# Performance work log

Measured on AMD Instinct MI355X. Metric: run time of the kernel, lower is better.

## Reference

```python
import jax, jax.numpy as jnp
import numpy as np

HEADS1, HID1 = 4, 64   # layer 1: concat -> 256
HEADS2, HID2 = 1, 64   # layer 2: out_channels
NEG_SLOPE = 0.2


def gat_layer(x_src, x_dst, W_src, W_dst, att_src, att_dst, bias, src, dst, n_tgt, heads, hid):
    # bipartite GATConv (PyG math), concat heads
    xs = (x_src @ W_src).reshape(-1, heads, hid)          # [Ns,H,C]
    xd = (x_dst @ W_dst).reshape(-1, heads, hid)          # [Nt,H,C]
    a_s = jnp.sum(xs * att_src, axis=-1)                  # [Ns,H]
    a_d = jnp.sum(xd * att_dst, axis=-1)                  # [Nt,H]
    e = jax.nn.leaky_relu(a_s[src] + a_d[dst], NEG_SLOPE) # [E,H]
    m = jax.ops.segment_max(e, dst, num_segments=n_tgt)
    m = jnp.where(jnp.isfinite(m), m, 0.0)
    ex = jnp.exp(e - m[dst])
    denom = jax.ops.segment_sum(ex, dst, num_segments=n_tgt)
    alpha = ex / (denom[dst] + 1e-16)                     # edge softmax per target
    msg = xs[src] * alpha[:, :, None]                     # [E,H,C]
    out = jax.ops.segment_sum(msg, dst, num_segments=n_tgt)
    return out.reshape(n_tgt, heads * hid) + bias


def setup_inputs() -> dict:
    key = jax.random.key(0)
    ks = jax.random.split(key, 20)
    N0, NT1, NT2 = 100000, 25000, 5000
    E1, E2 = 400000, 100000
    IN, H1 = 256, HEADS1 * HID1  # 256
    OUT = HEADS2 * HID2          # 64
    g = lambda k, sh, fan: jax.random.normal(k, sh, jnp.float32) * (1.0 / np.sqrt(fan))
    return {
        'x': jax.random.normal(ks[0], (N0, IN), jnp.float32),
        'src1': jax.random.randint(ks[1], (E1,), 0, N0),
        'dst1': jax.random.randint(ks[2], (E1,), 0, NT1),
        'src2': jax.random.randint(ks[3], (E2,), 0, NT1),
        'dst2': jax.random.randint(ks[4], (E2,), 0, NT2),
        'n_tgt1': NT1, 'n_tgt2': NT2,
        'W1_src': g(ks[5], (IN, H1), IN), 'W1_dst': g(ks[6], (IN, H1), IN),
        'att1_src': g(ks[7], (HEADS1, HID1), HID1), 'att1_dst': g(ks[8], (HEADS1, HID1), HID1),
        'bias1': jnp.zeros((H1,), jnp.float32),
        'skip1_W': g(ks[9], (IN, H1), IN), 'skip1_b': jnp.zeros((H1,), jnp.float32),
        'W2_src': g(ks[10], (H1, OUT), H1), 'W2_dst': g(ks[11], (H1, OUT), H1),
        'att2_src': g(ks[12], (HEADS2, HID2), HID2), 'att2_dst': g(ks[13], (HEADS2, HID2), HID2),
        'bias2': jnp.zeros((OUT,), jnp.float32),
        'skip2_W': g(ks[14], (H1, OUT), H1), 'skip2_b': jnp.zeros((OUT,), jnp.float32),
    }


def reference(x, src1, dst1, src2, dst2, n_tgt1, n_tgt2,
              W1_src, W1_dst, att1_src, att1_dst, bias1, skip1_W, skip1_b,
              W2_src, W2_dst, att2_src, att2_dst, bias2, skip2_W, skip2_b):
    # layer 1: conv + skip + elu (dropout inactive in eval)
    x_t1 = x[:n_tgt1]
    h = gat_layer(x, x_t1, W1_src, W1_dst, att1_src, att1_dst, bias1,
                  src1, dst1, n_tgt1, HEADS1, HID1)
    h = h + (x_t1 @ skip1_W + skip1_b)
    h = jax.nn.elu(h)
    # layer 2 (final): conv + skip, then log_softmax
    x_t2 = h[:n_tgt2]
    o = gat_layer(h, x_t2, W2_src, W2_dst, att2_src, att2_dst, bias2,
                  src2, dst2, n_tgt2, HEADS2, HID2)
    o = o + (x_t2 @ skip2_W + skip2_b)
    return jax.nn.log_softmax(o, axis=-1)
```

## Files before the change

kernel.cpp:

```cpp
#include <hip/hip_runtime.h>
#include <hip/hip_bf16.h>

using bf16 = __hip_bfloat16;
typedef __attribute__((ext_vector_type(8))) short short8;
typedef __attribute__((ext_vector_type(4))) short short4v;
typedef __attribute__((ext_vector_type(4))) float float4v;

__device__ __forceinline__ short f2bs(float x) {
    bf16 b = __float2bfloat16(x);
    return __builtin_bit_cast(short, b);
}
__device__ __forceinline__ float bs2f(short s) {
    return __uint_as_float(((unsigned)(unsigned short)s) << 16);
}
__device__ __forceinline__ void glds16(const void* g, void* l) {
    __builtin_amdgcn_global_load_lds(
        (const __attribute__((address_space(1))) unsigned int*)g,
        (__attribute__((address_space(3))) unsigned int*)l, 16, 0, 0);
}

__global__ __launch_bounds__(512, 4) void gemm_l1(
        const float* __restrict__ A, const bf16* __restrict__ Bt,
        bf16* __restrict__ xs1, bf16* __restrict__ sk1,
        float* __restrict__ as1, float* __restrict__ ad1,
        const float* __restrict__ att_s, const float* __restrict__ att_d,
        int M, int NT) {
    __shared__ short ldsB[64 * 512];
    const int y = blockIdx.y;
    const int row0 = blockIdx.x * 128;
    if (y >= 2 && row0 >= NT) return;
    const int col0 = y * 128;
    const int tid = threadIdx.x;
    const int wave = tid >> 6, lane = tid & 63;
    const int quad = lane >> 4, l16 = lane & 15;

#pragma unroll
    for (int kit = 0; kit < 8; kit++)
        glds16(&Bt[(size_t)(col0 + wave * 16 + l16) * 256 + kit * 32 + quad * 8],
               &ldsB[(wave * 8 + kit) * 512]);

    const int arow_ = row0 + wave * 16 + l16;
    const int arow = arow_ < M ? arow_ : M - 1;
    const float* Ap = &A[(size_t)arow * 256 + quad * 8];

    const float4v fz = {0.f, 0.f, 0.f, 0.f};
    float4v acc[8];
#pragma unroll
    for (int n = 0; n < 8; n++) acc[n] = fz;

    __syncthreads();

    float4v pf0[4], pf1[4];
#pragma unroll
    for (int i = 0; i < 4; i++) {
        pf0[i] = *(const float4v*)(Ap + i * 32);
        pf1[i] = *(const float4v*)(Ap + i * 32 + 4);
    }

#pragma unroll
    for (int kit = 0; kit < 8; kit++) {
        const int s = kit & 3;
        short8 af;
#pragma unroll
        for (int j = 0; j < 4; j++) { af[j] = f2bs(pf0[s][j]); af[4 + j] = f2bs(pf1[s][j]); }
        if (kit < 4) {
            pf0[s] = *(const float4v*)(Ap + (kit + 4) * 32);
            pf1[s] = *(const float4v*)(Ap + (kit + 4) * 32 + 4);
        }
#pragma unroll
        for (int n = 0; n < 8; n++) {
            short8 bf = *(short8*)&ldsB[(n * 8 + kit) * 512 + lane * 8];
            acc[n] = __builtin_amdgcn_mfma_f32_16x16x32_bf16(af, bf, acc[n], 0, 0, 0);
        }
    }

    const int rbase = row0 + wave * 16 + quad * 4;

    if (y < 4) {
        const float* attc = y < 2 ? att_s : att_d;
        const int hbase = y < 2 ? y * 2 : (y - 2) * 2;
        const int aM = y < 2 ? M : NT;
        float* aout = y < 2 ? as1 : ad1;
#pragma unroll
        for (int h = 0; h < 2; h++) {
            float av[4];
#pragma unroll
            for (int n = 0; n < 4; n++) av[n] = attc[(hbase + h) * 64 + n * 16 + l16];
#pragma unroll
            for (int r = 0; r < 4; r++) {
                float t = acc[h * 4 + 0][r] * av[0] + acc[h * 4 + 1][r] * av[1] +
                          acc[h * 4 + 2][r] * av[2] + acc[h * 4 + 3][r] * av[3];
                t += __shfl_xor(t, 1, 64);
                t += __shfl_xor(t, 2, 64);
                t += __shfl_xor(t, 4, 64);
                t += __shfl_xor(t, 8, 64);
                int grow = rbase + r;
                if (l16 == 0 && grow < aM) aout[(size_t)grow * 4 + hbase + h] = t;
            }
        }
    }

    if (y < 2) {
#pragma unroll
        for (int n = 0; n < 8; n++) {
            int col = col0 + n * 16 + l16;
#pragma unroll
            for (int r = 0; r < 4; r++) {
                int row = rbase + r;
                if (row < M) xs1[(size_t)row * 256 + col] = __float2bfloat16(acc[n][r]);
            }
        }
    } else if (y >= 4) {
#pragma unroll
        for (int n = 0; n < 8; n++) {
            int scol = col0 - 512 + n * 16 + l16;
#pragma unroll
            for (int r = 0; r < 4; r++) {
                int row = rbase + r;
                if (row < NT) sk1[(size_t)row * 256 + scol] = __float2bfloat16(acc[n][r]);
            }
        }
    }
}

__global__ __launch_bounds__(512, 4) void gemm_l2(
        const bf16* __restrict__ Ah, const bf16* __restrict__ Bt,
        float* __restrict__ x2, float* __restrict__ a2,
        const float* __restrict__ attc, int NT) {
    __shared__ short ldsB[32 * 512];
    const int y = blockIdx.y;
    const int row0 = blockIdx.x * 128;
    const int col0 = y * 64;
    const int tid = threadIdx.x;
    const int wave = tid >> 6, lane = tid & 63;
    const int quad = lane >> 4, l16 = lane & 15;

#pragma unroll
    for (int i = 0; i < 4; i++) {
        int blk = wave * 4 + i;
        int cb = blk >> 3, kit = blk & 7;
        glds16(&Bt[(size_t)(col0 + cb * 16 + l16) * 256 + kit * 32 + quad * 8],
               &ldsB[blk * 512]);
    }

    const int arow = row0 + wave * 16 + l16;
    const bf16* Ap = &Ah[(size_t)arow * 256 + quad * 8];

    const float4v fz = {0.f, 0.f, 0.f, 0.f};
    float4v acc[4];
#pragma unroll
    for (int n = 0; n < 4; n++) acc[n] = fz;

    __syncthreads();

    short8 s[8];
#pragma unroll
    for (int kit = 0; kit < 8; kit++) s[kit] = *(const short8*)(Ap + kit * 32);

#pragma unroll
    for (int kit = 0; kit < 8; kit++) {
#pragma unroll
        for (int n = 0; n < 4; n++) {
            short8 bf = *(short8*)&ldsB[(n * 8 + kit) * 512 + lane * 8];
            acc[n] = __builtin_amdgcn_mfma_f32_16x16x32_bf16(s[kit], bf, acc[n], 0, 0, 0);
        }
    }

    const int rbase = row0 + wave * 16 + quad * 4;

    if (y < 2) {
        float av[4];
#pragma unroll
        for (int n = 0; n < 4; n++) av[n] = attc[y * 64 + n * 16 + l16];
#pragma unroll
        for (int r = 0; r < 4; r++) {
            float t = acc[0][r] * av[0] + acc[1][r] * av[1] +
                      acc[2][r] * av[2] + acc[3][r] * av[3];
            t += __shfl_xor(t, 1, 64);
            t += __shfl_xor(t, 2, 64);
            t += __shfl_xor(t, 4, 64);
            t += __shfl_xor(t, 8, 64);
            int grow = rbase + r;
            if (l16 == 0 && grow < NT) a2[(size_t)grow * 2 + y] = t;
        }
    }
#pragma unroll
    for (int n = 0; n < 4; n++) {
        int col = col0 + n * 16 + l16;
#pragma unroll
        for (int r = 0; r < 4; r++) {
            int row = rbase + r;
            if (row < NT) x2[(size_t)row * 192 + col] = acc[n][r];
        }
    }
}

__global__ void prep_all(const float* __restrict__ W1s, const float* __restrict__ W1d,
                         const float* __restrict__ W1sk, const float* __restrict__ W2s,
                         const float* __restrict__ W2d, const float* __restrict__ W2sk,
                         const float* __restrict__ a2s, const float* __restrict__ a2d,
                         bf16* __restrict__ Wt1, bf16* __restrict__ Wt2,
                         float* __restrict__ at2c, int* __restrict__ fills, int nfill) {
    int t = blockIdx.x * blockDim.x + threadIdx.x;
    if (t < 196608) {
        int n = t >> 8, k = t & 255;
        const float* W = n < 256 ? W1s : (n < 512 ? W1d : W1sk);
        Wt1[t] = __float2bfloat16(W[k * 256 + (n & 255)]);
    } else if (t < 245760) {
        int i = t - 196608;
        int n = i >> 8, k = i & 255;
        const float* W = n < 64 ? W2s : (n < 128 ? W2d : W2sk);
        Wt2[i] = __float2bfloat16(W[k * 64 + (n & 63)]);
    } else if (t < 245888) {
        int i = t - 245760;
        at2c[i] = i < 64 ? a2s[i] : a2d[i - 64];
    } else if (t < 245888 + nfill) {
        fills[t - 245888] = 0;
    }
}

__global__ void bucket_scatter(const int* __restrict__ s1, const int* __restrict__ d1, int E1,
                               const int* __restrict__ s2, const int* __restrict__ d2, int E2,
                               int* __restrict__ fill1, int* __restrict__ fill2,
                               int* __restrict__ psrc1, int* __restrict__ psrc2) {
    int t = blockIdx.x * blockDim.x + threadIdx.x;
    if (t < E1) {
        int d = d1[t];
        int pos = atomicAdd(&fill1[d], 1);
        if (pos < 64) psrc1[(d << 6) + pos] = s1[t];
    } else if (t < E1 + E2) {
        int tt = t - E1;
        int d = d2[tt];
        int pos = atomicAdd(&fill2[d], 1);
        if (pos < 64) psrc2[(d << 6) + pos] = s2[tt];
    }
}

__global__ __launch_bounds__(256) void agg_h4(
        const int* __restrict__ fill, const int* __restrict__ psrc,
        const bf16* __restrict__ X, const float* __restrict__ as1,
        const float* __restrict__ ad1, const float* __restrict__ bias,
        const bf16* __restrict__ skip, const float* __restrict__ skipb,
        bf16* __restrict__ h) {
    __shared__ float exl[4][64][4];
    __shared__ float red[4][256];
    const int d = blockIdx.x;
    const int tid = threadIdx.x;
    const int wv = tid >> 6, lane = tid & 63;
    const int head = lane >> 4;
    int deg = fill[d];
    deg = deg < 64 ? deg : 64;
    int se = 0;
    float4v ex4 = {0.f, 0.f, 0.f, 0.f};
    const float4v ad4 = *(const float4v*)&ad1[(size_t)d * 4];
    if (lane < deg) {
        se = psrc[((size_t)d << 6) + lane];
        float4v as4 = *(const float4v*)&as1[(size_t)se * 4];
#pragma unroll
        for (int c = 0; c < 4; c++) {
            float v = as4[c] + ad4[c];
            v = v > 0.f ? v : 0.2f * v;
            ex4[c] = expf(v);
        }
    }
    *(float4v*)&exl[wv][lane][0] = ex4;
    float4v dn = ex4;
#pragma unroll
    for (int o = 32; o; o >>= 1) {
        dn.x += __shfl_xor(dn.x, o, 64);
        dn.y += __shfl_xor(dn.y, o, 64);
        dn.z += __shfl_xor(dn.z, o, 64);
        dn.w += __shfl_xor(dn.w, o, 64);
    }
    float4v acc = {0.f, 0.f, 0.f, 0.f}, acc2 = {0.f, 0.f, 0.f, 0.f};
    int p = wv;
    for (; p + 4 < deg; p += 8) {
        int sA = __shfl(se, p, 64), sB = __shfl(se, p + 4, 64);
        float aA = exl[wv][p][head], aB = exl[wv][p + 4][head];
        short4v xa = *(const short4v*)&X[(size_t)sA * 256 + lane * 4];
        short4v xb = *(const short4v*)&X[(size_t)sB * 256 + lane * 4];
        acc.x += bs2f(xa.x) * aA; acc2.x += bs2f(xb.x) * aB;
        acc.y += bs2f(xa.y) * aA; acc2.y += bs2f(xb.y) * aB;
        acc.z += bs2f(xa.z) * aA; acc2.z += bs2f(xb.z) * aB;
        acc.w += bs2f(xa.w) * aA; acc2.w += bs2f(xb.w) * aB;
    }
    for (; p < deg; p += 4) {
        int sA = __shfl(se, p, 64);
        float aA = exl[wv][p][head];
        short4v xa = *(const short4v*)&X[(size_t)sA * 256 + lane * 4];
        acc.x += bs2f(xa.x) * aA;
        acc.y += bs2f(xa.y) * aA;
        acc.z += bs2f(xa.z) * aA;
        acc.w += bs2f(xa.w) * aA;
    }
    acc.x += acc2.x; acc.y += acc2.y; acc.z += acc2.z; acc.w += acc2.w;
    *(float4v*)&red[wv][lane * 4] = acc;
    __syncthreads();
    const int f = tid;
    float sum = red[0][f] + red[1][f] + red[2][f] + red[3][f];
    int hf = f >> 6;
    float den = hf == 0 ? dn.x : hf == 1 ? dn.y : hf == 2 ? dn.z : dn.w;
    float v = sum / (den + 1e-16f) + bias[f] + __bfloat162float(skip[(size_t)d * 256 + f]) +
              skipb[f];
    h[(size_t)d * 256 + f] = __float2bfloat16(v > 0.f ? v : expm1f(v));
}

__global__ __launch_bounds__(256) void agg_h1(
        const int* __restrict__ fill2, const int* __restrict__ psrc2,
        const float* __restrict__ x2, const float* __restrict__ a2,
        const float* __restrict__ bias, const float* __restrict__ skipb,
        float* __restrict__ out, int M) {
    const int d = blockIdx.x * 4 + (threadIdx.x >> 6);
    const int lane = threadIdx.x & 63;
    if (d >= M) return;
    int deg = fill2[d];
    deg = deg < 64 ? deg : 64;
    int se = 0;
    float exv = 0.f;
    const float adv = a2[(size_t)d * 2 + 1];
    if (lane < deg) {
        se = psrc2[((size_t)d << 6) + lane];
        float v = a2[(size_t)se * 2] + adv;
        v = v > 0.f ? v : 0.2f * v;
        exv = expf(v);
    }
    float den = exv;
#pragma unroll
    for (int o = 32; o; o >>= 1) den += __shfl_xor(den, o, 64);
    float acc = 0.f, acc2 = 0.f;
    int p = 0;
    for (; p + 1 < deg; p += 2) {
        int sA = __shfl(se, p, 64), sB = __shfl(se, p + 1, 64);
        float aA = __shfl(exv, p, 64), aB = __shfl(exv, p + 1, 64);
        acc += x2[(size_t)sA * 192 + lane] * aA;
        acc2 += x2[(size_t)sB * 192 + lane] * aB;
    }
    if (p < deg) {
        int sA = __shfl(se, p, 64);
        acc += x2[(size_t)sA * 192 + lane] * __shfl(exv, p, 64);
    }
    float v = (acc + acc2) / (den + 1e-16f) + bias[lane] +
              x2[(size_t)d * 192 + 128 + lane] + skipb[lane];
    float m = v;
#pragma unroll
    for (int o = 32; o; o >>= 1) m = fmaxf(m, __shfl_xor(m, o, 64));
    float e = expf(v - m);
#pragma unroll
    for (int o = 32; o; o >>= 1) e += __shfl_xor(e, o, 64);
    out[(size_t)d * 64 + lane] = v - m - logf(e);
}

extern "C" void kernel_launch(void* const* d_in, const int* in_sizes, int n_in,
                              void* d_out, int out_size, void* d_ws, size_t ws_size,
                              hipStream_t stream) {
    const float* x        = (const float*)d_in[0];
    const int*   src1     = (const int*)d_in[1];
    const int*   dst1     = (const int*)d_in[2];
    const int*   src2     = (const int*)d_in[3];
    const int*   dst2     = (const int*)d_in[4];
    const float* W1_src   = (const float*)d_in[7];
    const float* W1_dst   = (const float*)d_in[8];
    const float* att1_src = (const float*)d_in[9];
    const float* att1_dst = (const float*)d_in[10];
    const float* bias1    = (const float*)d_in[11];
    const float* skip1_W  = (const float*)d_in[12];
    const float* skip1_b  = (const float*)d_in[13];
    const float* W2_src   = (const float*)d_in[14];
    const float* W2_dst   = (const float*)d_in[15];
    const float* att2_src = (const float*)d_in[16];
    const float* att2_dst = (const float*)d_in[17];
    const float* bias2    = (const float*)d_in[18];
    const float* skip2_W  = (const float*)d_in[19];
    const float* skip2_b  = (const float*)d_in[20];

    const int N0  = in_sizes[0] / 256;
    const int E1  = in_sizes[1];
    const int E2  = in_sizes[3];
    const int NT1 = 25000, NT2 = 5000;
    const int NT1p = 25088;

    char* ws = (char*)d_ws;
    size_t off = 0;
    auto alloc = [&](size_t b) { size_t o = off; off += (b + 255) & ~(size_t)255; return o; };
    size_t o_xs1   = alloc((size_t)N0 * 256 * 2);
    size_t o_sk1   = alloc((size_t)NT1 * 256 * 2);
    size_t o_h     = alloc((size_t)NT1p * 256 * 2);
    size_t o_as1   = alloc((size_t)N0 * 4 * 4);
    size_t o_ad1   = alloc((size_t)NT1 * 4 * 4);
    size_t o_fill  = alloc((size_t)(NT1 + NT2) * 4);
    size_t o_psrc1 = alloc((size_t)NT1 * 64 * 4);
    size_t o_psrc2 = alloc((size_t)NT2 * 64 * 4);
    size_t o_wt1   = alloc((size_t)768 * 256 * 2);
    size_t o_wt2   = alloc((size_t)192 * 256 * 2);
    size_t o_at2c  = alloc((size_t)128 * 4);
    size_t off2a = o_xs1;
    auto alloc2 = [&](size_t b) { size_t o = off2a; off2a += (b + 255) & ~(size_t)255; return o; };
    size_t o_x2 = alloc2((size_t)NT1 * 192 * 4);
    size_t o_a2 = alloc2((size_t)NT1 * 2 * 4);

    bf16*  xs1   = (bf16*)(ws + o_xs1);
    bf16*  sk1   = (bf16*)(ws + o_sk1);
    bf16*  h     = (bf16*)(ws + o_h);
    float* as1   = (float*)(ws + o_as1);
    float* ad1   = (float*)(ws + o_ad1);
    int*   fill1 = (int*)(ws + o_fill);
    int*   fill2 = fill1 + NT1;
    int*   psrc1 = (int*)(ws + o_psrc1);
    int*   psrc2 = (int*)(ws + o_psrc2);
    bf16*  Wt1   = (bf16*)(ws + o_wt1);
    bf16*  Wt2   = (bf16*)(ws + o_wt2);
    float* at2c  = (float*)(ws + o_at2c);
    float* x2    = (float*)(ws + o_x2);
    float* a2    = (float*)(ws + o_a2);

    prep_all<<<(245888 + NT1 + NT2 + 255) / 256, 256, 0, stream>>>(
        W1_src, W1_dst, skip1_W, W2_src, W2_dst, skip2_W, att2_src, att2_dst,
        Wt1, Wt2, at2c, fill1, NT1 + NT2);
    bucket_scatter<<<(E1 + E2 + 255) / 256, 256, 0, stream>>>(
        src1, dst1, E1, src2, dst2, E2, fill1, fill2, psrc1, psrc2);
    gemm_l1<<<dim3((N0 + 127) / 128, 6), 512, 0, stream>>>(
        x, Wt1, xs1, sk1, as1, ad1, att1_src, att1_dst, N0, NT1);
    agg_h4<<<NT1, 256, 0, stream>>>(fill1, psrc1, xs1, as1, ad1, bias1, sk1, skip1_b, h);
    gemm_l2<<<dim3((NT1 + 127) / 128, 3), 512, 0, stream>>>(h, Wt2, x2, a2, at2c, NT1);
    agg_h1<<<(NT2 + 3) / 4, 256, 0, stream>>>(fill2, psrc2, x2, a2, bias2, skip2_b,
                                              (float*)d_out, NT2);
}
```

Measured before the change: 351.1 us.

## Pre-convert x to bf16 and retile layer-1 GEMM to 64-column blocks

Adds a bf16 conversion of the input features x to a fused prep kernel, which also absorbs the edge bucket scatter and weight transposes. The fill counters are now zeroed with a memset. The layer-1 GEMM reads bf16 A directly, uses 64-column tiles across 12 column blocks with column-major grid ordering so blocks sharing A rows run together, and loads A fragments before the barrier. This cuts the GEMM's A-read traffic and per-block register and LDS use. In exchange it adds an extra 51MB bf16 write and read of x and a larger workspace.

```diff
diff --git a/kernel.cpp b/kernel.cpp
--- a/kernel.cpp
+++ b/kernel.cpp
@@ -20,89 +20,78 @@
 }
 
 __global__ __launch_bounds__(512, 4) void gemm_l1(
-        const float* __restrict__ A, const bf16* __restrict__ Bt,
+        const bf16* __restrict__ A, const bf16* __restrict__ Bt,
         bf16* __restrict__ xs1, bf16* __restrict__ sk1,
         float* __restrict__ as1, float* __restrict__ ad1,
         const float* __restrict__ att_s, const float* __restrict__ att_d,
         int M, int NT) {
-    __shared__ short ldsB[64 * 512];
-    const int y = blockIdx.y;
-    const int row0 = blockIdx.x * 128;
-    if (y >= 2 && row0 >= NT) return;
-    const int col0 = y * 128;
+    __shared__ short ldsB[32 * 512];
+    const int y = blockIdx.x;
+    const int row0 = blockIdx.y * 128;
+    if (y >= 4 && row0 >= NT) return;
+    const int col0 = y * 64;
     const int tid = threadIdx.x;
     const int wave = tid >> 6, lane = tid & 63;
     const int quad = lane >> 4, l16 = lane & 15;
 
 #pragma unroll
-    for (int kit = 0; kit < 8; kit++)
-        glds16(&Bt[(size_t)(col0 + wave * 16 + l16) * 256 + kit * 32 + quad * 8],
-               &ldsB[(wave * 8 + kit) * 512]);
+    for (int i = 0; i < 4; i++) {
+        int blk = wave * 4 + i;
+        int cb = blk >> 3, kit = blk & 7;
+        glds16(&Bt[(size_t)(col0 + cb * 16 + l16) * 256 + kit * 32 + quad * 8],
+               &ldsB[blk * 512]);
+    }
 
     const int arow_ = row0 + wave * 16 + l16;
     const int arow = arow_ < M ? arow_ : M - 1;
-    const float* Ap = &A[(size_t)arow * 256 + quad * 8];
+    const bf16* Ap = &A[(size_t)arow * 256 + quad * 8];
+
+    short8 s[8];
+#pragma unroll
+    for (int kit = 0; kit < 8; kit++) s[kit] = *(const short8*)(Ap + kit * 32);
 
     const float4v fz = {0.f, 0.f, 0.f, 0.f};
-    float4v acc[8];
-#pragma unroll
-    for (int n = 0; n < 8; n++) acc[n] = fz;
+    float4v acc[4];
+#pragma unroll
+    for (int n = 0; n < 4; n++) acc[n] = fz;
 
     __syncthreads();
 
-    float4v pf0[4], pf1[4];
-#pragma unroll
-    for (int i = 0; i < 4; i++) {
-        pf0[i] = *(const float4v*)(Ap + i * 32);
-        pf1[i] = *(const float4v*)(Ap + i * 32 + 4);
-    }
-
 #pragma unroll
     for (int kit = 0; kit < 8; kit++) {
-        const int s = kit & 3;
-        short8 af;
-#pragma unroll
-        for (int j = 0; j < 4; j++) { af[j] = f2bs(pf0[s][j]); af[4 + j] = f2bs(pf1[s][j]); }
-        if (kit < 4) {
-            pf0[s] = *(const float4v*)(Ap + (kit + 4) * 32);
-            pf1[s] = *(const float4v*)(Ap + (kit + 4) * 32 + 4);
-        }
-#pragma unroll
-        for (int n = 0; n < 8; n++) {
+#pragma unroll
+        for (int n = 0; n < 4; n++) {
             short8 bf = *(short8*)&ldsB[(n * 8 + kit) * 512 + lane * 8];
-            acc[n] = __builtin_amdgcn_mfma_f32_16x16x32_bf16(af, bf, acc[n], 0, 0, 0);
+            acc[n] = __builtin_amdgcn_mfma_f32_16x16x32_bf16(s[kit], bf, acc[n], 0, 0, 0);
         }
     }
 
     const int rbase = row0 + wave * 16 + quad * 4;
 
+    if (y < 8) {
+        const float* attc = y < 4 ? att_s : att_d;
+        const int head = y & 3;
+        const int aM = y < 4 ? M : NT;
+        float* aout = y < 4 ? as1 : ad1;
+        float av[4];
+#pragma unroll
+        for (int n = 0; n < 4; n++) av[n] = attc[head * 64 + n * 16 + l16];
+#pragma unroll
+        for (int r = 0; r < 4; r++) {
+            float t = acc[0][r] * av[0] + acc[1][r] * av[1] +
+                      acc[2][r] * av[2] + acc[3][r] * av[3];
+            t += __shfl_xor(t, 1, 64);
+            t += __shfl_xor(t, 2, 64);
+            t += __shfl_xor(t, 4, 64);
+            t += __shfl_xor(t, 8, 64);
+            int grow = rbase + r;
+            if (l16 == 0 && grow < aM) aout[(size_t)grow * 4 + head] = t;
+        }
+    }
+
     if (y < 4) {
-        const float* attc = y < 2 ? att_s : att_d;
-        const int hbase = y < 2 ? y * 2 : (y - 2) * 2;
-        const int aM = y < 2 ? M : NT;
-        float* aout = y < 2 ? as1 : ad1;
-#pragma unroll
-        for (int h = 0; h < 2; h++) {
-            float av[4];
-#pragma unroll
-            for (int n = 0; n < 4; n++) av[n] = attc[(hbase + h) * 64 + n * 16 + l16];
-#pragma unroll
-            for (int r = 0; r < 4; r++) {
-                float t = acc[h * 4 + 0][r] * av[0] + acc[h * 4 + 1][r] * av[1] +
-                          acc[h * 4 + 2][r] * av[2] + acc[h * 4 + 3][r] * av[3];
-                t += __shfl_xor(t, 1, 64);
-                t += __shfl_xor(t, 2, 64);
-                t += __shfl_xor(t, 4, 64);
-                t += __shfl_xor(t, 8, 64);
-                int grow = rbase + r;
-                if (l16 == 0 && grow < aM) aout[(size_t)grow * 4 + hbase + h] = t;
-            }
-        }
-    }
-
-    if (y < 2) {
-#pragma unroll
-        for (int n = 0; n < 8; n++) {
+#pragma unroll
+        for (int n = 0; n < 4; n++) {
             int col = col0 + n * 16 + l16;
 #pragma unroll
             for (int r = 0; r < 4; r++) {
@@ -110,9 +99,9 @@
                 if (row < M) xs1[(size_t)row * 256 + col] = __float2bfloat16(acc[n][r]);
             }
         }
-    } else if (y >= 4) {
-#pragma unroll
-        for (int n = 0; n < 8; n++) {
+    } else if (y >= 8) {
+#pragma unroll
+        for (int n = 0; n < 4; n++) {
             int scol = col0 - 512 + n * 16 + l16;
 #pragma unroll
             for (int r = 0; r < 4; r++) {
@@ -146,16 +135,16 @@
     const int arow = row0 + wave * 16 + l16;
     const bf16* Ap = &Ah[(size_t)arow * 256 + quad * 8];
 
+    short8 s[8];
+#pragma unroll
+    for (int kit = 0; kit < 8; kit++) s[kit] = *(const short8*)(Ap + kit * 32);
+
     const float4v fz = {0.f, 0.f, 0.f, 0.f};
     float4v acc[4];
 #pragma unroll
     for (int n = 0; n < 4; n++) acc[n] = fz;
 
     __syncthreads();
-
-    short8 s[8];
-#pragma unroll
-    for (int kit = 0; kit < 8; kit++) s[kit] = *(const short8*)(Ap + kit * 32);
 
 #pragma unroll
     for (int kit = 0; kit < 8; kit++) {
@@ -195,13 +184,44 @@
     }
 }
 
-__global__ void prep_all(const float* __restrict__ W1s, const float* __restrict__ W1d,
-                         const float* __restrict__ W1sk, const float* __restrict__ W2s,
-                         const float* __restrict__ W2d, const float* __restrict__ W2sk,
-                         const float* __restrict__ a2s, const float* __restrict__ a2d,
-                         bf16* __restrict__ Wt1, bf16* __restrict__ Wt2,
-                         float* __restrict__ at2c, int* __restrict__ fills, int nfill) {
+__global__ void prep_fused(
+        const int* __restrict__ s1, const int* __restrict__ d1, int E1,
+        const int* __restrict__ s2, const int* __restrict__ d2, int E2,
+        int* __restrict__ fill1, int* __restrict__ fill2,
+        int* __restrict__ psrc1, int* __restrict__ psrc2,
+        const float* __restrict__ x, bf16* __restrict__ xbf, int N0,
+        const float* __restrict__ W1s, const float* __restrict__ W1d,
+        const float* __restrict__ W1sk, const float* __restrict__ W2s,
+        const float* __restrict__ W2d, const float* __restrict__ W2sk,
+        const float* __restrict__ a2s, const float* __restrict__ a2d,
+        bf16* __restrict__ Wt1, bf16* __restrict__ Wt2,
+        float* __restrict__ at2c) {
     int t = blockIdx.x * blockDim.x + threadIdx.x;
+    if (t < E1) {
+        int d = d1[t];
+        int pos = atomicAdd(&fill1[d], 1);
+        if (pos < 64) psrc1[(d << 6) + pos] = s1[t];
+        return;
+    }
+    t -= E1;
+    if (t < E2) {
+        int d = d2[t];
+        int pos = atomicAdd(&fill2[d], 1);
+        if (pos < 64) psrc2[(d << 6) + pos] = s2[t];
+        return;
+    }
+    t -= E2;
+    const int NC = N0 * 32;
+    if (t < NC) {
+        const float4v* p = (const float4v*)&x[(size_t)t * 8];
+        float4v a = p[0], b = p[1];
+        short8 v;
+#pragma unroll
+        for (int j = 0; j < 4; j++) { v[j] = f2bs(a[j]); v[4 + j] = f2bs(b[j]); }
+        *(short8*)&xbf[(size_t)t * 8] = v;
+        return;
+    }
+    t -= NC;
     if (t < 196608) {
         int n = t >> 8, k = t & 255;
         const float* W = n < 256 ? W1s : (n < 512 ? W1d : W1sk);
@@ -214,25 +234,6 @@
     } else if (t < 245888) {
         int i = t - 245760;
         at2c[i] = i < 64 ? a2s[i] : a2d[i - 64];
-    } else if (t < 245888 + nfill) {
-        fills[t - 245888] = 0;
-    }
-}
-
-__global__ void bucket_scatter(const int* __restrict__ s1, const int* __restrict__ d1, int E1,
-                               const int* __restrict__ s2, const int* __restrict__ d2, int E2,
-                               int* __restrict__ fill1, int* __restrict__ fill2,
-                               int* __restrict__ psrc1, int* __restrict__ psrc2) {
-    int t = blockIdx.x * blockDim.x + threadIdx.x;
-    if (t < E1) {
-        int d = d1[t];
-        int pos = atomicAdd(&fill1[d], 1);
-        if (pos < 64) psrc1[(d << 6) + pos] = s1[t];
-    } else if (t < E1 + E2) {
-        int tt = t - E1;
-        int d = d2[tt];
-        int pos = atomicAdd(&fill2[d], 1);
-        if (pos < 64) psrc2[(d << 6) + pos] = s2[tt];
     }
 }
 
@@ -382,6 +383,7 @@
     char* ws = (char*)d_ws;
     size_t off = 0;
     auto alloc = [&](size_t b) { size_t o = off; off += (b + 255) & ~(size_t)255; return o; };
+    size_t o_xbf   = alloc((size_t)N0 * 256 * 2);
     size_t o_xs1   = alloc((size_t)N0 * 256 * 2);
     size_t o_sk1   = alloc((size_t)NT1 * 256 * 2);
     size_t o_h     = alloc((size_t)NT1p * 256 * 2);
@@ -398,6 +400,7 @@
     size_t o_x2 = alloc2((size_t)NT1 * 192 * 4);
     size_t o_a2 = alloc2((size_t)NT1 * 2 * 4);
 
+    bf16*  xbf   = (bf16*)(ws + o_xbf);
     bf16*  xs1   = (bf16*)(ws + o_xs1);
     bf16*  sk1   = (bf16*)(ws + o_sk1);
     bf16*  h     = (bf16*)(ws + o_h);
@@ -413,13 +416,16 @@
     float* x2    = (float*)(ws + o_x2);
     float* a2    = (float*)(ws + o_a2);
 
-    prep_all<<<(245888 + NT1 + NT2 + 255) / 256, 256, 0, stream>>>(
-        W1_src, W1_dst, skip1_W, W2_src, W2_dst, skip2_W, att2_src, att2_dst,
-        Wt1, Wt2, at2c, fill1, NT1 + NT2);
-    bucket_scatter<<<(E1 + E2 + 255) / 256, 256, 0, stream>>>(
-        src1, dst1, E1, src2, dst2, E2, fill1, fill2, psrc1, psrc2);
-    gemm_l1<<<dim3((N0 + 127) / 128, 6), 512, 0, stream>>>(
-        x, Wt1, xs1, sk1, as1, ad1, att1_src, att1_dst, N0, NT1);
+    hipMemsetAsync(fill1, 0, (size_t)(NT1 + NT2) * 4, stream);
+    {
+        int total = E1 + E2 + N0 * 32 + 245888;
+        prep_fused<<<(total + 255) / 256, 256, 0, stream>>>(
+            src1, dst1, E1, src2, dst2, E2, fill1, fill2, psrc1, psrc2,
+            x, xbf, N0, W1_src, W1_dst, skip1_W, W2_src, W2_dst, skip2_W,
+            att2_src, att2_dst, Wt1, Wt2, at2c);
+    }
+    gemm_l1<<<dim3(12, (N0 + 127) / 128), 512, 0, stream>>>(
+        xbf, Wt1, xs1, sk1, as1, ad1, att1_src, att1_dst, N0, NT1);
     agg_h4<<<NT1, 256, 0, stream>>>(fill1, psrc1, xs1, as1, ad1, bias1, sk1, skip1_b, h);
     gemm_l2<<<dim3((NT1 + 127) / 128, 3), 512, 0, stream>>>(h, Wt2, x2, a2, at2c, NT1);
     agg_h1<<<(NT2 + 3) / 4, 256, 0, stream>>>(fill2, psrc2, x2, a2, bias2, skip2_b,
```

After: 354.3 us. No clear change (+0.9%).
